# Kernel tuning notes

Measured on AMD Instinct MI355X. Metric: run time of the kernel, lower is better.

## Reference

```python
import jax, jax.numpy as jnp
import numpy as np

EPS = 1e-5          # InstanceNorm eps (torch default)
KERNEL = 25         # moving_avg_kernel_size
TAU = 1.0           # gumbel softmax temperature
REGIME_NUM = 8


def _inorm(x):
    # InstanceNorm1d without affine on (N, C, L): normalize over last dim (biased var)
    m = x.mean(-1, keepdims=True)
    v = ((x - m) ** 2).mean(-1, keepdims=True)
    return (x - m) * jax.lax.rsqrt(v + EPS)


def _lbr(x, W, b):
    # Linear -> InstanceNorm (over last dim) -> exact GELU
    return jax.nn.gelu(_inorm(x @ W + b), approximate=False)


def _moving_avg(x, k):
    # x: (B, L, C); edge-replicate pad (k-1)//2 on both sides, sliding mean via cumsum
    p = (k - 1) // 2
    xp = jnp.concatenate([jnp.repeat(x[:, :1], p, axis=1), x,
                          jnp.repeat(x[:, -1:], p, axis=1)], axis=1)
    cs = jnp.concatenate([jnp.zeros_like(xp[:, :1]), jnp.cumsum(xp, axis=1)], axis=1)
    return (cs[:, k:] - cs[:, :-k]) / k  # (B, L, C)


def _encode(x, Ws, bs, Wt, bt):
    # inputs - inputs[:, 0:1]; series decomposition; seasonal+trend branches
    x = x - x[:, :1]
    mm = _moving_avg(x, KERNEL)
    return _lbr(x - mm, Ws, bs) + _lbr(mm, Wt, bt)  # (B, L, H)


def reference(inputs_longterm, inputs_shortterm,
              Ws, bs, Wt, bt,
              Wh1, bh1, Wl1, bl1, Wh2, bh2, Wl2, bl2, Wh3, bh3, Wl3, bl3,
              Wr, br, proto):
    e_lt = _encode(inputs_longterm, Ws, bs, Wt, bt)   # (B, L_lt, H)
    e_st = _encode(inputs_shortterm, Ws, bs, Wt, bt)  # (B, L_st, H)

    # RegimeEncoder: alternate hidden-dim and lookback-dim LinearBatchRelu layers
    o = _lbr(e_lt, Wh1, bh1)
    o = jnp.swapaxes(_lbr(jnp.swapaxes(o, 1, 2), Wl1, bl1), 1, 2)
    o = _lbr(o, Wh2, bh2)
    o = jnp.swapaxes(_lbr(jnp.swapaxes(o, 1, 2), Wl2, bl2), 1, 2)
    o = _lbr(o, Wh3, bh3)
    o = jnp.swapaxes(_lbr(jnp.swapaxes(o, 1, 2), Wl3, bl3), 1, 2)  # (B, L_lt//8, H)
    logits = o.reshape(o.shape[0], -1) @ Wr + br  # (B, R)

    # gumbel_softmax(hard=True) with straight-through estimator
    g = jax.random.gumbel(jax.random.key(42), logits.shape, logits.dtype)
    y_soft = jax.nn.softmax((logits + g) / TAU, axis=-1)
    y_hard = jax.nn.one_hot(jnp.argmax(y_soft, axis=-1), REGIME_NUM, dtype=logits.dtype)
    w = y_hard - jax.lax.stop_gradient(y_soft) + y_soft  # (B, R)

    # weighted sum over regime prototypes, then combine with encoded shortterm
    sel = jnp.einsum('br,rnhmo->bnhmo', w, proto)          # (B, L_st, H, M, 3)
    out = jnp.einsum('bnh,bnhmo->bmo', e_st, sel)          # (B, M, 3)
    B = out.shape[0]
    return jax.nn.softmax(out.reshape(B, -1), axis=-1).reshape(out.shape)


def setup_inputs() -> dict:
    key = jax.random.key(0)
    ks = jax.random.split(key, 24)
    B, L_lt, L_st, C, H, R, M = 32, 512, 128, 9, 128, 8, 64
    s = 0.02
    d = {
        'inputs_longterm':  jax.random.normal(ks[0], (B, L_lt, C), jnp.float32),
        'inputs_shortterm': jax.random.normal(ks[1], (B, L_st, C), jnp.float32),
        'Ws': jax.random.normal(ks[2], (C, H), jnp.float32) * s,
        'bs': jnp.zeros((H,), jnp.float32),
        'Wt': jax.random.normal(ks[3], (C, H), jnp.float32) * s,
        'bt': jnp.zeros((H,), jnp.float32),
        'Wh1': jax.random.normal(ks[4], (H, H), jnp.float32) * s,
        'bh1': jnp.zeros((H,), jnp.float32),
        'Wl1': jax.random.normal(ks[5], (L_lt, L_lt // 2), jnp.float32) * s,
        'bl1': jnp.zeros((L_lt // 2,), jnp.float32),
        'Wh2': jax.random.normal(ks[6], (H, H), jnp.float32) * s,
        'bh2': jnp.zeros((H,), jnp.float32),
        'Wl2': jax.random.normal(ks[7], (L_lt // 2, L_lt // 4), jnp.float32) * s,
        'bl2': jnp.zeros((L_lt // 4,), jnp.float32),
        'Wh3': jax.random.normal(ks[8], (H, H), jnp.float32) * s,
        'bh3': jnp.zeros((H,), jnp.float32),
        'Wl3': jax.random.normal(ks[9], (L_lt // 4, L_lt // 8), jnp.float32) * s,
        'bl3': jnp.zeros((L_lt // 8,), jnp.float32),
        'Wr': jax.random.normal(ks[10], (H * L_lt // 8, R), jnp.float32) * s,
        'br': jnp.zeros((R,), jnp.float32),
        'proto': jax.random.normal(ks[11], (R, L_st, H, M, 3), jnp.float32),
    }
    return d
```

## Files before the change

### kernel.cpp

```cpp
#include <hip/hip_runtime.h>
#include <math.h>

#define EPS 1e-5f

__device__ __forceinline__ float gelu_exact(float x) {
    return 0.5f * x * (1.0f + erff(x * 0.7071067811865476f));
}

__device__ float block_sum(float v, float* red) {
    int lane = threadIdx.x & 63, wid = threadIdx.x >> 6;
#pragma unroll
    for (int off = 32; off > 0; off >>= 1) v += __shfl_down(v, off, 64);
    if (lane == 0) red[wid] = v;
    __syncthreads();
    int nw = ((int)blockDim.x + 63) >> 6;
    float s = red[0];
    for (int w = 1; w < nw; w++) s += red[w];
    __syncthreads();
    return s;
}

__device__ float block_max(float v, float* red) {
    int lane = threadIdx.x & 63, wid = threadIdx.x >> 6;
#pragma unroll
    for (int off = 32; off > 0; off >>= 1) v = fmaxf(v, __shfl_down(v, off, 64));
    if (lane == 0) red[wid] = v;
    __syncthreads();
    int nw = ((int)blockDim.x + 63) >> 6;
    float s = red[0];
    for (int w = 1; w < nw; w++) s = fmaxf(s, red[w]);
    __syncthreads();
    return s;
}

__device__ void threefry2x32(unsigned k0, unsigned k1, unsigned x0, unsigned x1,
                             unsigned& o0, unsigned& o1) {
    unsigned ks[3] = {k0, k1, k0 ^ k1 ^ 0x1BD11BDAu};
    const unsigned rot[2][4] = {{13u, 15u, 26u, 6u}, {17u, 29u, 16u, 24u}};
    x0 += ks[0]; x1 += ks[1];
#pragma unroll
    for (int i = 0; i < 5; i++) {
#pragma unroll
        for (int j = 0; j < 4; j++) {
            unsigned r = rot[i & 1][j];
            x0 += x1;
            x1 = (x1 << r) | (x1 >> (32 - r));
            x1 ^= x0;
        }
        x0 += ks[(i + 1) % 3];
        x1 += ks[(i + 2) % 3] + (unsigned)(i + 1);
    }
    o0 = x0; o1 = x1;
}

__device__ float gumbel_at(int j) {
    unsigned o0, o1;
    threefry2x32(0u, 42u, 0u, (unsigned)j, o0, o1);
    unsigned bits = o0 ^ o1;
    float f = __uint_as_float((bits >> 9) | 0x3F800000u) - 1.0f;
    float u = fmaxf(f + 1.17549435e-38f, 1.17549435e-38f);
    return -logf(-logf(u));
}

__global__ __launch_bounds__(256) void encode_kernel(
    const float* __restrict__ x_lt, const float* __restrict__ x_st,
    const float* __restrict__ Ws, const float* __restrict__ bs,
    const float* __restrict__ Wt, const float* __restrict__ bt,
    float* __restrict__ e_lt, float* __restrict__ e_st) {
    const int b = blockIdx.y;
    const int w = threadIdx.x >> 6, ln = threadIdx.x & 63;
    const float* x; float* e; int L, l;
    if (blockIdx.x < 128) { x = x_lt; e = e_lt; L = 512; l = blockIdx.x * 4 + w; }
    else { x = x_st; e = e_st; L = 128; l = (blockIdx.x - 128) * 4 + w; }
    __shared__ float xw_all[4][228];
    __shared__ float sm_all[4][20];
    float* xw = xw_all[w];
    float* sm = sm_all[w];
    const float* xb = x + (size_t)b * L * 9;
#pragma unroll
    for (int q = 0; q < 4; q++) {
        int f = ln + 64 * q;
        if (f < 225) {
            int row = f / 9, c = f - row * 9;
            int rr = l - 12 + row;
            rr = rr < 0 ? 0 : (rr >= L ? L - 1 : rr);
            xw[f] = xb[(size_t)rr * 9 + c];
        }
    }
    __syncthreads();
    if (ln < 9) {
        float s = 0.f;
#pragma unroll
        for (int j = 0; j < 25; j++) s += xw[j * 9 + ln];
        float x0 = xb[ln];
        float mm = (s - 25.f * x0) * (1.0f / 25.0f);
        sm[ln] = (xw[108 + ln] - x0) - mm;
        sm[ln + 10] = mm;
    }
    __syncthreads();
    float ysA = bs[ln], ysB = bs[ln + 64];
    float ytA = bt[ln], ytB = bt[ln + 64];
#pragma unroll
    for (int c = 0; c < 9; c++) {
        float sv = sm[c], mv = sm[c + 10];
        ysA += sv * Ws[c * 128 + ln];
        ysB += sv * Ws[c * 128 + ln + 64];
        ytA += mv * Wt[c * 128 + ln];
        ytB += mv * Wt[c * 128 + ln + 64];
    }
    float sa = ysA + ysB, sb2 = ytA + ytB;
#pragma unroll
    for (int off = 32; off > 0; off >>= 1) {
        sa += __shfl_xor(sa, off, 64);
        sb2 += __shfl_xor(sb2, off, 64);
    }
    float ms = sa * (1.0f / 128.0f), mt = sb2 * (1.0f / 128.0f);
    float dA = ysA - ms, dB = ysB - ms;
    float tA = ytA - mt, tB = ytB - mt;
    float qa = dA * dA + dB * dB, qb = tA * tA + tB * tB;
#pragma unroll
    for (int off = 32; off > 0; off >>= 1) {
        qa += __shfl_xor(qa, off, 64);
        qb += __shfl_xor(qb, off, 64);
    }
    float inva = rsqrtf(qa * (1.0f / 128.0f) + EPS);
    float invb = rsqrtf(qb * (1.0f / 128.0f) + EPS);
    float* eo = e + ((size_t)b * L + l) * 128;
    eo[ln] = gelu_exact(dA * inva) + gelu_exact(tA * invb);
    eo[ln + 64] = gelu_exact(dB * inva) + gelu_exact(tB * invb);
}

template <int K, int N, int WR, int KC, bool TRANS>
__global__ __launch_bounds__(256) void lbr_wave(
    const float* __restrict__ A, int S, int ABOFF,
    const float* __restrict__ W, const float* __restrict__ bias,
    float* __restrict__ out, int OROWS, int OBOFF) {
    constexpr int CG = N / 4;
    constexpr int SG = 64 / CG;
    constexpr int RW = SG * WR;
    constexpr int MT = 4 * RW;
    constexpr int LOG2MT = (MT == 8) ? 3 : ((MT == 16) ? 4 : 5);
    constexpr int WSZ = KC * N;
    constexpr int ASZ = 4 * RW * K;
    static_assert(WSZ >= MT * (N + 4), "TRANS tile must fit in W region");
    static_assert((WSZ / 4) % 256 == 0, "W chunk loads must be exact");
    __shared__ __align__(16) float lds[WSZ + ASZ];
    const int t = threadIdx.x;
    const int w = t >> 6, ln = t & 63;
    const int sg = ln / CG;
    const int n0 = (ln % CG) * 4;
    const int b = blockIdx.y;
    const int r0b = blockIdx.x * MT;
    const int r0w = r0b + w * RW;
    float* Wl = lds;
    float* As = lds + WSZ + w * RW * K;
    const float* Ab = A + (size_t)b * ABOFF;
    for (int idx = ln; idx < RW * (K / 4); idx += 64) {
        int rr = idx / (K / 4), kk = idx % (K / 4);
        float4 v = *(const float4*)(Ab + (size_t)(r0w + rr) * S + kk * 4);
        *(float4*)(As + rr * K + kk * 4) = v;
    }
    float4 acc[WR];
    {
        float4 bv = *(const float4*)(bias + n0);
#pragma unroll
        for (int j = 0; j < WR; j++) acc[j] = bv;
    }
    const float* ap = As + (sg * WR) * K;
    for (int kc0 = 0; kc0 < K; kc0 += KC) {
        __syncthreads();
        {
            const float4* wg = (const float4*)(W + (size_t)kc0 * N);
            float4* wl4 = (float4*)Wl;
#pragma unroll
            for (int i = 0; i < WSZ / 4 / 256; i++)
                wl4[t + i * 256] = wg[t + i * 256];
        }
        __syncthreads();
#pragma unroll 2
        for (int k = 0; k < KC; k += 4) {
            const float* wp = Wl + k * N + n0;
            float4 w0 = *(const float4*)(wp);
            float4 w1 = *(const float4*)(wp + N);
            float4 w2 = *(const float4*)(wp + 2 * N);
            float4 w3 = *(const float4*)(wp + 3 * N);
#pragma unroll
            for (int j = 0; j < WR; j++) {
                float4 a4 = *(const float4*)(ap + j * K + kc0 + k);
                acc[j].x += a4.x * w0.x; acc[j].y += a4.x * w0.y;
                acc[j].z += a4.x * w0.z; acc[j].w += a4.x * w0.w;
                acc[j].x += a4.y * w1.x; acc[j].y += a4.y * w1.y;
                acc[j].z += a4.y * w1.z; acc[j].w += a4.y * w1.w;
                acc[j].x += a4.z * w2.x; acc[j].y += a4.z * w2.y;
                acc[j].z += a4.z * w2.z; acc[j].w += a4.z * w2.w;
                acc[j].x += a4.w * w3.x; acc[j].y += a4.w * w3.y;
                acc[j].z += a4.w * w3.z; acc[j].w += a4.w * w3.w;
            }
        }
    }
    float4 res[WR];
#pragma unroll
    for (int j = 0; j < WR; j++) {
        float s = acc[j].x + acc[j].y + acc[j].z + acc[j].w;
#pragma unroll
        for (int off = CG / 2; off > 0; off >>= 1) s += __shfl_xor(s, off, 64);
        float m = s * (1.0f / (float)N);
        float dx = acc[j].x - m, dy = acc[j].y - m, dz = acc[j].z - m, dw = acc[j].w - m;
        float q = dx * dx + dy * dy + dz * dz + dw * dw;
#pragma unroll
        for (int off = CG / 2; off > 0; off >>= 1) q += __shfl_xor(q, off, 64);
        float inv = rsqrtf(q * (1.0f / (float)N) + EPS);
        res[j].x = gelu_exact(dx * inv);
        res[j].y = gelu_exact(dy * inv);
        res[j].z = gelu_exact(dz * inv);
        res[j].w = gelu_exact(dw * inv);
    }
    if constexpr (TRANS) {
        __syncthreads();
#pragma unroll
        for (int j = 0; j < WR; j++) {
            int rl = w * RW + sg * WR + j;
            *(float4*)(lds + rl * (N + 4) + n0) = res[j];
        }
        __syncthreads();
        float* ob = out + (size_t)b * OBOFF + r0b;
        for (int e = t; e < MT * N; e += 256) {
            int r = e & (MT - 1), n = e >> LOG2MT;
            ob[(size_t)n * OROWS + r] = lds[r * (N + 4) + n];
        }
    } else {
        float* ob = out + (size_t)b * OBOFF;
#pragma unroll
        for (int j = 0; j < WR; j++) {
            int row = r0w + sg * WR + j;
            *(float4*)(ob + (size_t)row * N + n0) = res[j];
        }
    }
}

__global__ __launch_bounds__(256) void logits_select(
    const float* __restrict__ O6, const float* __restrict__ Wr,
    const float* __restrict__ br, float* __restrict__ sel_w, int* __restrict__ sel_r) {
    int b = blockIdx.x, t = threadIdx.x;
    __shared__ float sO6[128 * 68];
    __shared__ float red[4][8];
    const float4* ob4 = (const float4*)(O6 + (size_t)b * 8192);
    for (int i4 = t; i4 < 2048; i4 += 256) {
        float4 v = ob4[i4];
        int p = i4 * 4;
        int h = p >> 6, l4 = p & 63;
        *(float4*)(&sO6[h * 68 + l4]) = v;
    }
    __syncthreads();
    float acc[8] = {0, 0, 0, 0, 0, 0, 0, 0};
#pragma unroll 4
    for (int q = 0; q < 32; q++) {
        int i = q * 256 + t;
        int l4 = i >> 7, h = i & 127;
        float v = sO6[h * 68 + l4];
        const float4* wr = (const float4*)(Wr + (size_t)i * 8);
        float4 w0 = wr[0], w1 = wr[1];
        acc[0] += v * w0.x; acc[1] += v * w0.y; acc[2] += v * w0.z; acc[3] += v * w0.w;
        acc[4] += v * w1.x; acc[5] += v * w1.y; acc[6] += v * w1.z; acc[7] += v * w1.w;
    }
#pragma unroll
    for (int j = 0; j < 8; j++)
#pragma unroll
        for (int off = 32; off > 0; off >>= 1) acc[j] += __shfl_xor(acc[j], off, 64);
    int lane = t & 63, wid = t >> 6;
    if (lane == 0)
        for (int j = 0; j < 8; j++) red[wid][j] = acc[j];
    __syncthreads();
    if (t == 0) {
        float z[8];
        for (int j = 0; j < 8; j++) {
            float lg = br[j] + red[0][j] + red[1][j] + red[2][j] + red[3][j];
            z[j] = lg + gumbel_at(b * 8 + j);
        }
        int am = 0;
        float zm = z[0];
        for (int j = 1; j < 8; j++)
            if (z[j] > zm) { zm = z[j]; am = j; }
        float ssum = 0.f;
        for (int j = 0; j < 8; j++) ssum += expf(z[j] - zm);
        float s = 1.0f / ssum;
        sel_w[b] = (1.0f - s) + s;
        sel_r[b] = am;
    }
}

__global__ __launch_bounds__(192, 4) void einsum_nsplit(
    const float* __restrict__ e_st, const float* __restrict__ proto,
    const int* __restrict__ sel_r, float* __restrict__ part) {
    const int n = blockIdx.x, r = blockIdx.y, hz = blockIdx.z, t = threadIdx.x;
    const int w = t >> 6, ln = t & 63;
    const int rg = ln >> 4;
    const int q4 = (w * 16 + (ln & 15)) * 4;
    __shared__ int loc[32];
    __shared__ int s_gs;
    if (t == 0) {
        int g = 0;
        for (int bb = 0; bb < 32; bb++)
            if (sel_r[bb] == r) loc[g++] = bb;
        s_gs = g;
    }
    __syncthreads();
    const int gs = s_gs;
    if (gs == 0) return;
    __shared__ __align__(16) float es[64][12];
    const float* pb = proto + (((size_t)r * 128 + n) * 128 + hz * 64) * 192;
    float* po = part + (size_t)hz * (32 * 128 * 192);
    for (int s0 = 0; s0 < gs; s0 += 8) {
        int np = gs - s0 < 8 ? gs - s0 : 8;
        __syncthreads();
        for (int i = t; i < 512; i += 192) {
            int sb = i >> 6, h = i & 63;
            float v = 0.f;
            if (sb < np)
                v = e_st[((size_t)loc[s0 + sb] * 128 + n) * 128 + hz * 64 + h];
            es[h][sb] = v;
        }
        __syncthreads();
        float4 a[8];
#pragma unroll
        for (int sb = 0; sb < 8; sb++) a[sb] = make_float4(0.f, 0.f, 0.f, 0.f);
#pragma unroll 4
        for (int hh = 0; hh < 16; hh++) {
            int row = hh * 4 + rg;
            float4 pv = *(const float4*)(pb + (size_t)row * 192 + q4);
            float4 e0 = *(const float4*)(&es[row][0]);
            float4 e1 = *(const float4*)(&es[row][4]);
#define ACC4(j, s) a[j].x += (s) * pv.x; a[j].y += (s) * pv.y; \
                   a[j].z += (s) * pv.z; a[j].w += (s) * pv.w;
            ACC4(0, e0.x) ACC4(1, e0.y) ACC4(2, e0.z) ACC4(3, e0.w)
            ACC4(4, e1.x) ACC4(5, e1.y) ACC4(6, e1.z) ACC4(7, e1.w)
#undef ACC4
        }
#pragma unroll
        for (int sb = 0; sb < 8; sb++) {
            a[sb].x += __shfl_xor(a[sb].x, 16, 64);
            a[sb].y += __shfl_xor(a[sb].y, 16, 64);
            a[sb].z += __shfl_xor(a[sb].z, 16, 64);
            a[sb].w += __shfl_xor(a[sb].w, 16, 64);
            a[sb].x += __shfl_xor(a[sb].x, 32, 64);
            a[sb].y += __shfl_xor(a[sb].y, 32, 64);
            a[sb].z += __shfl_xor(a[sb].z, 32, 64);
            a[sb].w += __shfl_xor(a[sb].w, 32, 64);
        }
        if (ln < 16) {
#pragma unroll
            for (int sb = 0; sb < 8; sb++) {
                if (sb < np) {
                    int bb = loc[s0 + sb];
                    *(float4*)(po + ((size_t)bb * 128 + n) * 192 + q4) = a[sb];
                }
            }
        }
    }
}

__global__ void finalize_kernel(const float* __restrict__ part, const float* __restrict__ sel_w,
                                float* __restrict__ out) {
    int b = blockIdx.x, t = threadIdx.x;
    __shared__ float red[4];
    const float* p0 = part + (size_t)b * 128 * 192 + t;
    const float* p1 = p0 + (size_t)32 * 128 * 192;
    float v = 0.f;
#pragma unroll 8
    for (int c = 0; c < 128; c++) {
        v += p0[(size_t)c * 192];
        v += p1[(size_t)c * 192];
    }
    v *= sel_w[b];
    float mx = block_max(v, red);
    float e = expf(v - mx);
    float s = block_sum(e, red);
    out[(size_t)b * 192 + t] = e / s;
}

extern "C" void kernel_launch(void* const* d_in, const int* in_sizes, int n_in,
                              void* d_out, int out_size, void* d_ws, size_t ws_size,
                              hipStream_t stream) {
    const float* in_lt = (const float*)d_in[0];
    const float* in_st = (const float*)d_in[1];
    const float* Ws  = (const float*)d_in[2];  const float* bs  = (const float*)d_in[3];
    const float* Wt  = (const float*)d_in[4];  const float* bt  = (const float*)d_in[5];
    const float* Wh1 = (const float*)d_in[6];  const float* bh1 = (const float*)d_in[7];
    const float* Wl1 = (const float*)d_in[8];  const float* bl1 = (const float*)d_in[9];
    const float* Wh2 = (const float*)d_in[10]; const float* bh2 = (const float*)d_in[11];
    const float* Wl2 = (const float*)d_in[12]; const float* bl2 = (const float*)d_in[13];
    const float* Wh3 = (const float*)d_in[14]; const float* bh3 = (const float*)d_in[15];
    const float* Wl3 = (const float*)d_in[16]; const float* bl3 = (const float*)d_in[17];
    const float* Wr  = (const float*)d_in[18]; const float* br  = (const float*)d_in[19];
    const float* proto = (const float*)d_in[20];
    float* out = (float*)d_out;

    float* ws = (float*)d_ws;
    size_t off = 0;
    float* e_lt = ws + off; off += (size_t)32 * 512 * 128;
    float* e_st = ws + off; off += (size_t)32 * 128 * 128;
    float* O1T = ws + off; off += (size_t)128 * 16384;
    float* O2T = ws + off; off += (size_t)256 * 4096;
    float* O3T = ws + off; off += (size_t)128 * 8192;
    float* O4T = ws + off; off += (size_t)128 * 4096;
    float* O5T = ws + off; off += (size_t)128 * 4096;
    float* O6 = ws + off; off += (size_t)32 * 128 * 64;
    float* part = ws + off; off += (size_t)2 * 32 * 128 * 192;
    float* sel_w = ws + off; off += 32;
    int* sel_r = (int*)(ws + off); off += 32;

    encode_kernel<<<dim3(160, 32), 256, 0, stream>>>(in_lt, in_st, Ws, bs, Wt, bt, e_lt, e_st);
    lbr_wave<128, 128, 2, 64, true><<<dim3(1024, 1), 256, 0, stream>>>(
        e_lt, 128, 0, Wh1, bh1, O1T, 16384, 0);
    lbr_wave<512, 256, 2, 32, true><<<dim3(16, 32), 256, 0, stream>>>(
        O1T, 16384, 512, Wl1, bl1, O2T, 4096, 128);
    lbr_wave<128, 128, 2, 64, true><<<dim3(16, 32), 256, 0, stream>>>(
        O2T, 4096, 128, Wh2, bh2, O3T, 8192, 256);
    lbr_wave<256, 128, 1, 64, true><<<dim3(16, 32), 256, 0, stream>>>(
        O3T, 8192, 256, Wl2, bl2, O4T, 4096, 128);
    lbr_wave<128, 128, 1, 64, true><<<dim3(16, 32), 256, 0, stream>>>(
        O4T, 4096, 128, Wh3, bh3, O5T, 4096, 128);
    lbr_wave<128, 64, 1, 128, false><<<dim3(8, 32), 256, 0, stream>>>(
        O5T, 4096, 128, Wl3, bl3, O6, 0, 8192);
    logits_select<<<32, 256, 0, stream>>>(O6, Wr, br, sel_w, sel_r);
    einsum_nsplit<<<dim3(128, 8, 2), 192, 0, stream>>>(e_st, proto, sel_r, part);
    finalize_kernel<<<32, 192, 0, stream>>>(part, sel_w, out);
}
```

Baseline: 321.8 us.

## Fuse regime-encoder layer chain into one cooperative kernel with grid syncs

```diff
diff --git a/kernel.cpp b/kernel.cpp
--- a/kernel.cpp
+++ b/kernel.cpp
@@ -1,5 +1,8 @@
 #include <hip/hip_runtime.h>
+#include <hip/hip_cooperative_groups.h>
 #include <math.h>
+
+namespace cg = cooperative_groups;
 
 #define EPS 1e-5f
 
@@ -131,7 +134,8 @@
 }
 
 template <int K, int N, int WR, int KC, bool TRANS>
-__global__ __launch_bounds__(256) void lbr_wave(
+__device__ void lbr_layer(
+    float* lds, int unit, int UX,
     const float* __restrict__ A, int S, int ABOFF,
     const float* __restrict__ W, const float* __restrict__ bias,
     float* __restrict__ out, int OROWS, int OBOFF) {
@@ -141,16 +145,15 @@
     constexpr int MT = 4 * RW;
     constexpr int LOG2MT = (MT == 8) ? 3 : ((MT == 16) ? 4 : 5);
     constexpr int WSZ = KC * N;
-    constexpr int ASZ = 4 * RW * K;
     static_assert(WSZ >= MT * (N + 4), "TRANS tile must fit in W region");
     static_assert((WSZ / 4) % 256 == 0, "W chunk loads must be exact");
-    __shared__ __align__(16) float lds[WSZ + ASZ];
+    static_assert(WSZ + 4 * RW * K <= 12288, "fits shared lds arena");
     const int t = threadIdx.x;
     const int w = t >> 6, ln = t & 63;
     const int sg = ln / CG;
     const int n0 = (ln % CG) * 4;
-    const int b = blockIdx.y;
-    const int r0b = blockIdx.x * MT;
+    const int bx = unit % UX, b = unit / UX;
+    const int r0b = bx * MT;
     const int r0w = r0b + w * RW;
     float* Wl = lds;
     float* As = lds + WSZ + w * RW * K;
@@ -238,54 +241,82 @@
     }
 }
 
-__global__ __launch_bounds__(256) void logits_select(
-    const float* __restrict__ O6, const float* __restrict__ Wr,
-    const float* __restrict__ br, float* __restrict__ sel_w, int* __restrict__ sel_r) {
-    int b = blockIdx.x, t = threadIdx.x;
-    __shared__ float sO6[128 * 68];
-    __shared__ float red[4][8];
-    const float4* ob4 = (const float4*)(O6 + (size_t)b * 8192);
-    for (int i4 = t; i4 < 2048; i4 += 256) {
-        float4 v = ob4[i4];
-        int p = i4 * 4;
-        int h = p >> 6, l4 = p & 63;
-        *(float4*)(&sO6[h * 68 + l4]) = v;
-    }
-    __syncthreads();
-    float acc[8] = {0, 0, 0, 0, 0, 0, 0, 0};
+__global__ __launch_bounds__(256) void chain_kernel(
+    const float* __restrict__ e_lt,
+    const float* __restrict__ Wh1, const float* __restrict__ bh1,
+    const float* __restrict__ Wl1, const float* __restrict__ bl1,
+    const float* __restrict__ Wh2, const float* __restrict__ bh2,
+    const float* __restrict__ Wl2, const float* __restrict__ bl2,
+    const float* __restrict__ Wh3, const float* __restrict__ bh3,
+    const float* __restrict__ Wl3, const float* __restrict__ bl3,
+    const float* __restrict__ Wr, const float* __restrict__ br,
+    float* __restrict__ O1T, float* __restrict__ O2T, float* __restrict__ O3T,
+    float* __restrict__ O4T, float* __restrict__ O5T, float* __restrict__ O6,
+    float* __restrict__ sel_w, int* __restrict__ sel_r) {
+    __shared__ __align__(16) float lds[12288];
+    __shared__ float redl[4][8];
+    cg::grid_group grid = cg::this_grid();
+    const int blk = blockIdx.x;
+    lbr_layer<128, 128, 2, 64, true>(lds, blk, 1024, e_lt, 128, 0, Wh1, bh1, O1T, 16384, 0);
+    lbr_layer<128, 128, 2, 64, true>(lds, blk + 512, 1024, e_lt, 128, 0, Wh1, bh1, O1T, 16384, 0);
+    grid.sync();
+    lbr_layer<512, 256, 2, 32, true>(lds, blk, 16, O1T, 16384, 512, Wl1, bl1, O2T, 4096, 128);
+    grid.sync();
+    lbr_layer<128, 128, 2, 64, true>(lds, blk, 16, O2T, 4096, 128, Wh2, bh2, O3T, 8192, 256);
+    grid.sync();
+    lbr_layer<256, 128, 1, 64, true>(lds, blk, 16, O3T, 8192, 256, Wl2, bl2, O4T, 4096, 128);
+    grid.sync();
+    lbr_layer<128, 128, 1, 64, true>(lds, blk, 16, O4T, 4096, 128, Wh3, bh3, O5T, 4096, 128);
+    grid.sync();
+    if (blk < 256)
+        lbr_layer<128, 64, 1, 128, false>(lds, blk, 8, O5T, 4096, 128, Wl3, bl3, O6, 0, 8192);
+    grid.sync();
+    if (blk < 32) {
+        const int b = blk, t = threadIdx.x;
+        float* sO6 = lds;
+        const float4* ob4 = (const float4*)(O6 + (size_t)b * 8192);
+        for (int i4 = t; i4 < 2048; i4 += 256) {
+            float4 v = ob4[i4];
+            int p = i4 * 4;
+            int h = p >> 6, l4 = p & 63;
+            *(float4*)(&sO6[h * 68 + l4]) = v;
+        }
+        __syncthreads();
+        float acc[8] = {0, 0, 0, 0, 0, 0, 0, 0};
 #pragma unroll 4
-    for (int q = 0; q < 32; q++) {
-        int i = q * 256 + t;
-        int l4 = i >> 7, h = i & 127;
-        float v = sO6[h * 68 + l4];
-        const float4* wr = (const float4*)(Wr + (size_t)i * 8);
-        float4 w0 = wr[0], w1 = wr[1];
-        acc[0] += v * w0.x; acc[1] += v * w0.y; acc[2] += v * w0.z; acc[3] += v * w0.w;
-        acc[4] += v * w1.x; acc[5] += v * w1.y; acc[6] += v * w1.z; acc[7] += v * w1.w;
-    }
-#pragma unroll
-    for (int j = 0; j < 8; j++)
-#pragma unroll
-        for (int off = 32; off > 0; off >>= 1) acc[j] += __shfl_xor(acc[j], off, 64);
-    int lane = t & 63, wid = t >> 6;
-    if (lane == 0)
-        for (int j = 0; j < 8; j++) red[wid][j] = acc[j];
-    __syncthreads();
-    if (t == 0) {
-        float z[8];
-        for (int j = 0; j < 8; j++) {
-            float lg = br[j] + red[0][j] + red[1][j] + red[2][j] + red[3][j];
-            z[j] = lg + gumbel_at(b * 8 + j);
-        }
-        int am = 0;
-        float zm = z[0];
-        for (int j = 1; j < 8; j++)
-            if (z[j] > zm) { zm = z[j]; am = j; }
-        float ssum = 0.f;
-        for (int j = 0; j < 8; j++) ssum += expf(z[j] - zm);
-        float s = 1.0f / ssum;
-        sel_w[b] = (1.0f - s) + s;
-        sel_r[b] = am;
+        for (int q = 0; q < 32; q++) {
+            int i = q * 256 + t;
+            int l4 = i >> 7, h = i & 127;
+            float v = sO6[h * 68 + l4];
+            const float4* wr = (const float4*)(Wr + (size_t)i * 8);
+            float4 w0 = wr[0], w1 = wr[1];
+            acc[0] += v * w0.x; acc[1] += v * w0.y; acc[2] += v * w0.z; acc[3] += v * w0.w;
+            acc[4] += v * w1.x; acc[5] += v * w1.y; acc[6] += v * w1.z; acc[7] += v * w1.w;
+        }
+#pragma unroll
+        for (int j = 0; j < 8; j++)
+#pragma unroll
+            for (int off = 32; off > 0; off >>= 1) acc[j] += __shfl_xor(acc[j], off, 64);
+        int lane = t & 63, wid = t >> 6;
+        if (lane == 0)
+            for (int j = 0; j < 8; j++) redl[wid][j] = acc[j];
+        __syncthreads();
+        if (t == 0) {
+            float z[8];
+            for (int j = 0; j < 8; j++) {
+                float lg = br[j] + redl[0][j] + redl[1][j] + redl[2][j] + redl[3][j];
+                z[j] = lg + gumbel_at(b * 8 + j);
+            }
+            int am = 0;
+            float zm = z[0];
+            for (int j = 1; j < 8; j++)
+                if (z[j] > zm) { zm = z[j]; am = j; }
+            float ssum = 0.f;
+            for (int j = 0; j < 8; j++) ssum += expf(z[j] - zm);
+            float s = 1.0f / ssum;
+            sel_w[b] = (1.0f - s) + s;
+            sel_r[b] = am;
+        }
     }
 }
 
@@ -410,19 +441,18 @@
     int* sel_r = (int*)(ws + off); off += 32;
 
     encode_kernel<<<dim3(160, 32), 256, 0, stream>>>(in_lt, in_st, Ws, bs, Wt, bt, e_lt, e_st);
-    lbr_wave<128, 128, 2, 64, true><<<dim3(1024, 1), 256, 0, stream>>>(
-        e_lt, 128, 0, Wh1, bh1, O1T, 16384, 0);
-    lbr_wave<512, 256, 2, 32, true><<<dim3(16, 32), 256, 0, stream>>>(
-        O1T, 16384, 512, Wl1, bl1, O2T, 4096, 128);
-    lbr_wave<128, 128, 2, 64, true><<<dim3(16, 32), 256, 0, stream>>>(
-        O2T, 4096, 128, Wh2, bh2, O3T, 8192, 256);
-    lbr_wave<256, 128, 1, 64, true><<<dim3(16, 32), 256, 0, stream>>>(
-        O3T, 8192, 256, Wl2, bl2, O4T, 4096, 128);
-    lbr_wave<128, 128, 1, 64, true><<<dim3(16, 32), 256, 0, stream>>>(
-        O4T, 4096, 128, Wh3, bh3, O5T, 4096, 128);
-    lbr_wave<128, 64, 1, 128, false><<<dim3(8, 32), 256, 0, stream>>>(
-        O5T, 4096, 128, Wl3, bl3, O6, 0, 8192);
-    logits_select<<<32, 256, 0, stream>>>(O6, Wr, br, sel_w, sel_r);
+
+    void* args[] = {
+        (void*)&e_lt,
+        (void*)&Wh1, (void*)&bh1, (void*)&Wl1, (void*)&bl1,
+        (void*)&Wh2, (void*)&bh2, (void*)&Wl2, (void*)&bl2,
+        (void*)&Wh3, (void*)&bh3, (void*)&Wl3, (void*)&bl3,
+        (void*)&Wr, (void*)&br,
+        (void*)&O1T, (void*)&O2T, (void*)&O3T, (void*)&O4T, (void*)&O5T,
+        (void*)&O6, (void*)&sel_w, (void*)&sel_r};
+    hipLaunchCooperativeKernel(reinterpret_cast<void*>(chain_kernel),
+                               dim3(512), dim3(256), args, 0, stream);
+
     einsum_nsplit<<<dim3(128, 8, 2), 192, 0, stream>>>(e_st, proto, sel_r, part);
     finalize_kernel<<<32, 192, 0, stream>>>(part, sel_w, out);
 }
```

Result: slower. 677.8 us (+110.6%).

## Fuse long-term encoder into first hidden LBR and Wl3 layer into logits

Applied to the files above, without the earlier changes.

```diff
diff --git a/kernel.cpp b/kernel.cpp
--- a/kernel.cpp
+++ b/kernel.cpp
@@ -62,21 +62,20 @@
     return -logf(-logf(u));
 }
 
-__global__ __launch_bounds__(256) void encode_kernel(
-    const float* __restrict__ x_lt, const float* __restrict__ x_st,
+__global__ __launch_bounds__(256) void encode_st_kernel(
+    const float* __restrict__ x_st,
     const float* __restrict__ Ws, const float* __restrict__ bs,
     const float* __restrict__ Wt, const float* __restrict__ bt,
-    float* __restrict__ e_lt, float* __restrict__ e_st) {
+    float* __restrict__ e_st) {
     const int b = blockIdx.y;
     const int w = threadIdx.x >> 6, ln = threadIdx.x & 63;
-    const float* x; float* e; int L, l;
-    if (blockIdx.x < 128) { x = x_lt; e = e_lt; L = 512; l = blockIdx.x * 4 + w; }
-    else { x = x_st; e = e_st; L = 128; l = (blockIdx.x - 128) * 4 + w; }
+    const int L = 128;
+    const int l = blockIdx.x * 4 + w;
     __shared__ float xw_all[4][228];
     __shared__ float sm_all[4][20];
     float* xw = xw_all[w];
     float* sm = sm_all[w];
-    const float* xb = x + (size_t)b * L * 9;
+    const float* xb = x_st + (size_t)b * L * 9;
 #pragma unroll
     for (int q = 0; q < 4; q++) {
         int f = ln + 64 * q;
@@ -125,9 +124,157 @@
     }
     float inva = rsqrtf(qa * (1.0f / 128.0f) + EPS);
     float invb = rsqrtf(qb * (1.0f / 128.0f) + EPS);
-    float* eo = e + ((size_t)b * L + l) * 128;
+    float* eo = e_st + ((size_t)b * L + l) * 128;
     eo[ln] = gelu_exact(dA * inva) + gelu_exact(tA * invb);
     eo[ln + 64] = gelu_exact(dB * inva) + gelu_exact(tB * invb);
+}
+
+__global__ __launch_bounds__(256) void enc_h1(
+    const float* __restrict__ x_lt,
+    const float* __restrict__ Ws, const float* __restrict__ bs,
+    const float* __restrict__ Wt, const float* __restrict__ bt,
+    const float* __restrict__ Wh1, const float* __restrict__ bh1,
+    float* __restrict__ O1T) {
+    constexpr int K = 128, N = 128, WR = 2, KC = 64;
+    constexpr int CG = N / 4;
+    constexpr int SG = 64 / CG;
+    constexpr int RW = SG * WR;
+    constexpr int MT = 16;
+    constexpr int WSZ = KC * N;
+    __shared__ __align__(16) float lds[WSZ + MT * K];
+    __shared__ float xwin[40 * 9];
+    __shared__ float x0s[9];
+    __shared__ float smS[16 * 9], smT[16 * 9];
+    const int t = threadIdx.x;
+    const int w = t >> 6, ln = t & 63;
+    const int bx = blockIdx.x;
+    const int b = bx >> 5;
+    const int l0 = (bx & 31) * 16;
+    const float* xb = x_lt + (size_t)b * 512 * 9;
+    for (int f = t; f < 360; f += 256) {
+        int row = f / 9, c = f - row * 9;
+        int rr = l0 - 12 + row;
+        rr = rr < 0 ? 0 : (rr > 511 ? 511 : rr);
+        xwin[f] = xb[(size_t)rr * 9 + c];
+    }
+    if (t < 9) x0s[t] = xb[t];
+    __syncthreads();
+    if (t < 144) {
+        int li = t / 9, c = t - (t / 9) * 9;
+        float s = 0.f;
+#pragma unroll
+        for (int j = 0; j < 25; j++) s += xwin[(li + j) * 9 + c];
+        float x0 = x0s[c];
+        float mm = (s - 25.f * x0) * (1.0f / 25.0f);
+        smS[t] = (xwin[(li + 12) * 9 + c] - x0) - mm;
+        smT[t] = mm;
+    }
+    __syncthreads();
+    float* As = lds + WSZ;
+    for (int q = 0; q < 4; q++) {
+        int li = w * 4 + q;
+        const float* sS = smS + li * 9;
+        const float* sT = smT + li * 9;
+        float ysA = bs[ln], ysB = bs[ln + 64];
+        float ytA = bt[ln], ytB = bt[ln + 64];
+#pragma unroll
+        for (int c = 0; c < 9; c++) {
+            float sv = sS[c], mv = sT[c];
+            ysA += sv * Ws[c * 128 + ln];
+            ysB += sv * Ws[c * 128 + ln + 64];
+            ytA += mv * Wt[c * 128 + ln];
+            ytB += mv * Wt[c * 128 + ln + 64];
+        }
+        float sa = ysA + ysB, sb2 = ytA + ytB;
+#pragma unroll
+        for (int off = 32; off > 0; off >>= 1) {
+            sa += __shfl_xor(sa, off, 64);
+            sb2 += __shfl_xor(sb2, off, 64);
+        }
+        float ms = sa * (1.0f / 128.0f), mt = sb2 * (1.0f / 128.0f);
+        float dA = ysA - ms, dB = ysB - ms;
+        float tA = ytA - mt, tB = ytB - mt;
+        float qa = dA * dA + dB * dB, qb = tA * tA + tB * tB;
+#pragma unroll
+        for (int off = 32; off > 0; off >>= 1) {
+            qa += __shfl_xor(qa, off, 64);
+            qb += __shfl_xor(qb, off, 64);
+        }
+        float inva = rsqrtf(qa * (1.0f / 128.0f) + EPS);
+        float invb = rsqrtf(qb * (1.0f / 128.0f) + EPS);
+        As[li * 128 + ln] = gelu_exact(dA * inva) + gelu_exact(tA * invb);
+        As[li * 128 + ln + 64] = gelu_exact(dB * inva) + gelu_exact(tB * invb);
+    }
+    __syncthreads();
+    const int sg = ln / CG;
+    const int n0 = (ln % CG) * 4;
+    float4 acc[WR];
+    {
+        float4 bv = *(const float4*)(bh1 + n0);
+#pragma unroll
+        for (int j = 0; j < WR; j++) acc[j] = bv;
+    }
+    const float* ap = As + (w * RW + sg * WR) * K;
+    for (int kc0 = 0; kc0 < K; kc0 += KC) {
+        if (kc0) __syncthreads();
+        {
+            const float4* wg = (const float4*)(Wh1 + (size_t)kc0 * N);
+            float4* wl4 = (float4*)lds;
+#pragma unroll
+            for (int i = 0; i < WSZ / 4 / 256; i++)
+                wl4[t + i * 256] = wg[t + i * 256];
+        }
+        __syncthreads();
+#pragma unroll 2
+        for (int k = 0; k < KC; k += 4) {
+            const float* wp = lds + k * N + n0;
+            float4 w0 = *(const float4*)(wp);
+            float4 w1 = *(const float4*)(wp + N);
+            float4 w2 = *(const float4*)(wp + 2 * N);
+            float4 w3 = *(const float4*)(wp + 3 * N);
+#pragma unroll
+            for (int j = 0; j < WR; j++) {
+                float4 a4 = *(const float4*)(ap + j * K + kc0 + k);
+                acc[j].x += a4.x * w0.x; acc[j].y += a4.x * w0.y;
+                acc[j].z += a4.x * w0.z; acc[j].w += a4.x * w0.w;
+                acc[j].x += a4.y * w1.x; acc[j].y += a4.y * w1.y;
+                acc[j].z += a4.y * w1.z; acc[j].w += a4.y * w1.w;
+                acc[j].x += a4.z * w2.x; acc[j].y += a4.z * w2.y;
+                acc[j].z += a4.z * w2.z; acc[j].w += a4.z * w2.w;
+                acc[j].x += a4.w * w3.x; acc[j].y += a4.w * w3.y;
+                acc[j].z += a4.w * w3.z; acc[j].w += a4.w * w3.w;
+            }
+        }
+    }
+    float4 res[WR];
+#pragma unroll
+    for (int j = 0; j < WR; j++) {
+        float s = acc[j].x + acc[j].y + acc[j].z + acc[j].w;
+#pragma unroll
+        for (int off = CG / 2; off > 0; off >>= 1) s += __shfl_xor(s, off, 64);
+        float m = s * (1.0f / (float)N);
+        float dx = acc[j].x - m, dy = acc[j].y - m, dz = acc[j].z - m, dw = acc[j].w - m;
+        float q = dx * dx + dy * dy + dz * dz + dw * dw;
+#pragma unroll
+        for (int off = CG / 2; off > 0; off >>= 1) q += __shfl_xor(q, off, 64);
+        float inv = rsqrtf(q * (1.0f / (float)N) + EPS);
+        res[j].x = gelu_exact(dx * inv);
+        res[j].y = gelu_exact(dy * inv);
+        res[j].z = gelu_exact(dz * inv);
+        res[j].w = gelu_exact(dw * inv);
+    }
+    __syncthreads();
+#pragma unroll
+    for (int j = 0; j < WR; j++) {
+        int rl = w * RW + sg * WR + j;
+        *(float4*)(lds + rl * (N + 4) + n0) = res[j];
+    }
+    __syncthreads();
+    float* ob = O1T + (size_t)bx * 16;
+    for (int e = t; e < MT * N; e += 256) {
+        int r = e & 15, n = e >> 4;
+        ob[(size_t)n * 16384 + r] = lds[r * (N + 4) + n];
+    }
 }
 
 template <int K, int N, int WR, int KC, bool TRANS>
@@ -238,43 +385,106 @@
     }
 }
 
-__global__ __launch_bounds__(256) void logits_select(
-    const float* __restrict__ O6, const float* __restrict__ Wr,
+__global__ __launch_bounds__(256) void l3_logits(
+    const float* __restrict__ O5T, const float* __restrict__ Wl3,
+    const float* __restrict__ bl3, const float* __restrict__ Wr,
     const float* __restrict__ br, float* __restrict__ sel_w, int* __restrict__ sel_r) {
-    int b = blockIdx.x, t = threadIdx.x;
-    __shared__ float sO6[128 * 68];
-    __shared__ float red[4][8];
-    const float4* ob4 = (const float4*)(O6 + (size_t)b * 8192);
-    for (int i4 = t; i4 < 2048; i4 += 256) {
-        float4 v = ob4[i4];
-        int p = i4 * 4;
-        int h = p >> 6, l4 = p & 63;
-        *(float4*)(&sO6[h * 68 + l4]) = v;
-    }
-    __syncthreads();
-    float acc[8] = {0, 0, 0, 0, 0, 0, 0, 0};
+    constexpr int N = 64, K = 128;
+    constexpr int CG = 16, WR = 8, RW = 32;
+    __shared__ __align__(16) float Wl[K * N];
+    __shared__ __align__(16) float As[128 * K];
+    __shared__ float redl[4][8];
+    const int t = threadIdx.x, w = t >> 6, ln = t & 63;
+    const int b = blockIdx.x;
+#pragma unroll
+    for (int i = 0; i < 16; i++) {
+        int idx = t + i * 256;
+        int rr = idx >> 5, kk = idx & 31;
+        *(float4*)(&As[rr * 128 + kk * 4]) =
+            *(const float4*)(O5T + (size_t)rr * 4096 + b * 128 + kk * 4);
+    }
+    {
+        const float4* wg = (const float4*)(Wl3);
+        float4* wl4 = (float4*)Wl;
+#pragma unroll
+        for (int i = 0; i < 8; i++) wl4[t + i * 256] = wg[t + i * 256];
+    }
+    __syncthreads();
+    const int sg = ln / CG;
+    const int n0 = (ln % CG) * 4;
+    const int row0 = w * RW + sg * WR;
+    float4 acc[WR];
+    {
+        float4 bv = *(const float4*)(bl3 + n0);
+#pragma unroll
+        for (int j = 0; j < WR; j++) acc[j] = bv;
+    }
+#pragma unroll 2
+    for (int k = 0; k < K; k += 4) {
+        const float* wp = Wl + k * N + n0;
+        float4 w0 = *(const float4*)(wp);
+        float4 w1 = *(const float4*)(wp + N);
+        float4 w2 = *(const float4*)(wp + 2 * N);
+        float4 w3 = *(const float4*)(wp + 3 * N);
+#pragma unroll
+        for (int j = 0; j < WR; j++) {
+            float4 a4 = *(const float4*)(&As[(row0 + j) * 128 + k]);
+            acc[j].x += a4.x * w0.x; acc[j].y += a4.x * w0.y;
+            acc[j].z += a4.x * w0.z; acc[j].w += a4.x * w0.w;
+            acc[j].x += a4.y * w1.x; acc[j].y += a4.y * w1.y;
+            acc[j].z += a4.y * w1.z; acc[j].w += a4.y * w1.w;
+            acc[j].x += a4.z * w2.x; acc[j].y += a4.z * w2.y;
+            acc[j].z += a4.z * w2.z; acc[j].w += a4.z * w2.w;
+            acc[j].x += a4.w * w3.x; acc[j].y += a4.w * w3.y;
+            acc[j].z += a4.w * w3.z; acc[j].w += a4.w * w3.w;
+        }
+    }
+    float4 res[WR];
+#pragma unroll
+    for (int j = 0; j < WR; j++) {
+        float s = acc[j].x + acc[j].y + acc[j].z + acc[j].w;
+#pragma unroll
+        for (int off = CG / 2; off > 0; off >>= 1) s += __shfl_xor(s, off, 64);
+        float m = s * (1.0f / (float)N);
+        float dx = acc[j].x - m, dy = acc[j].y - m, dz = acc[j].z - m, dw = acc[j].w - m;
+        float q = dx * dx + dy * dy + dz * dz + dw * dw;
+#pragma unroll
+        for (int off = CG / 2; off > 0; off >>= 1) q += __shfl_xor(q, off, 64);
+        float inv = rsqrtf(q * (1.0f / (float)N) + EPS);
+        res[j].x = gelu_exact(dx * inv);
+        res[j].y = gelu_exact(dy * inv);
+        res[j].z = gelu_exact(dz * inv);
+        res[j].w = gelu_exact(dw * inv);
+    }
+    __syncthreads();
+#pragma unroll
+    for (int j = 0; j < WR; j++) {
+        int row = row0 + j;
+        *(float4*)(&As[row * 68 + n0]) = res[j];
+    }
+    __syncthreads();
+    float acl[8] = {0, 0, 0, 0, 0, 0, 0, 0};
 #pragma unroll 4
     for (int q = 0; q < 32; q++) {
         int i = q * 256 + t;
         int l4 = i >> 7, h = i & 127;
-        float v = sO6[h * 68 + l4];
+        float v = As[h * 68 + l4];
         const float4* wr = (const float4*)(Wr + (size_t)i * 8);
         float4 w0 = wr[0], w1 = wr[1];
-        acc[0] += v * w0.x; acc[1] += v * w0.y; acc[2] += v * w0.z; acc[3] += v * w0.w;
-        acc[4] += v * w1.x; acc[5] += v * w1.y; acc[6] += v * w1.z; acc[7] += v * w1.w;
+        acl[0] += v * w0.x; acl[1] += v * w0.y; acl[2] += v * w0.z; acl[3] += v * w0.w;
+        acl[4] += v * w1.x; acl[5] += v * w1.y; acl[6] += v * w1.z; acl[7] += v * w1.w;
     }
 #pragma unroll
     for (int j = 0; j < 8; j++)
 #pragma unroll
-        for (int off = 32; off > 0; off >>= 1) acc[j] += __shfl_xor(acc[j], off, 64);
-    int lane = t & 63, wid = t >> 6;
-    if (lane == 0)
-        for (int j = 0; j < 8; j++) red[wid][j] = acc[j];
+        for (int off = 32; off > 0; off >>= 1) acl[j] += __shfl_xor(acl[j], off, 64);
+    if (ln == 0)
+        for (int j = 0; j < 8; j++) redl[w][j] = acl[j];
     __syncthreads();
     if (t == 0) {
         float z[8];
         for (int j = 0; j < 8; j++) {
-            float lg = br[j] + red[0][j] + red[1][j] + red[2][j] + red[3][j];
+            float lg = br[j] + redl[0][j] + redl[1][j] + redl[2][j] + redl[3][j];
             z[j] = lg + gumbel_at(b * 8 + j);
         }
         int am = 0;
@@ -408,10 +618,10 @@
     float* part = ws + off; off += (size_t)2 * 32 * 128 * 192;
     float* sel_w = ws + off; off += 32;
     int* sel_r = (int*)(ws + off); off += 32;
-
-    encode_kernel<<<dim3(160, 32), 256, 0, stream>>>(in_lt, in_st, Ws, bs, Wt, bt, e_lt, e_st);
-    lbr_wave<128, 128, 2, 64, true><<<dim3(1024, 1), 256, 0, stream>>>(
-        e_lt, 128, 0, Wh1, bh1, O1T, 16384, 0);
+    (void)e_lt; (void)O6;
+
+    encode_st_kernel<<<dim3(32, 32), 256, 0, stream>>>(in_st, Ws, bs, Wt, bt, e_st);
+    enc_h1<<<dim3(1024), 256, 0, stream>>>(in_lt, Ws, bs, Wt, bt, Wh1, bh1, O1T);
     lbr_wave<512, 256, 2, 32, true><<<dim3(16, 32), 256, 0, stream>>>(
         O1T, 16384, 512, Wl1, bl1, O2T, 4096, 128);
     lbr_wave<128, 128, 2, 64, true><<<dim3(16, 32), 256, 0, stream>>>(
@@ -420,9 +630,7 @@
         O3T, 8192, 256, Wl2, bl2, O4T, 4096, 128);
     lbr_wave<128, 128, 1, 64, true><<<dim3(16, 32), 256, 0, stream>>>(
         O4T, 4096, 128, Wh3, bh3, O5T, 4096, 128);
-    lbr_wave<128, 64, 1, 128, false><<<dim3(8, 32), 256, 0, stream>>>(
-        O5T, 4096, 128, Wl3, bl3, O6, 0, 8192);
-    logits_select<<<32, 256, 0, stream>>>(O6, Wr, br, sel_w, sel_r);
+    l3_logits<<<32, 256, 0, stream>>>(O5T, Wl3, bl3, Wr, br, sel_w, sel_r);
     einsum_nsplit<<<dim3(128, 8, 2), 192, 0, stream>>>(e_st, proto, sel_r, part);
     finalize_kernel<<<32, 192, 0, stream>>>(part, sel_w, out);
 }
```

Result: slower. 331.5 us (+3.0%).
